# Optimization experiments

Measured on AMD Instinct MI355X. Metric: run time of the kernel, lower is better.

The kernel has to match this reference:

```python
import jax, jax.numpy as jnp
import numpy as np

BN_EPS = 1e-5

def setup_inputs() -> dict:
    key = jax.random.key(0)
    k0, k1, k2, k3, k4 = jax.random.split(key, 5)
    B, N, D, E = 8, 256, 128, 4096
    x_l = jax.random.normal(k0, (B, N, D), dtype=jnp.float32)
    src = jax.random.randint(k1, (E,), 0, N)
    dst = jax.random.randint(k2, (E,), 0, N)
    edge_index_l = jnp.stack([src, dst], axis=0)  # [2, E]
    mask_l = jax.random.randint(k3, (B, N), 0, 2).astype(bool)
    W = jax.random.normal(k4, (D, D), dtype=jnp.float32) * (1.0 / np.sqrt(D))
    b = jnp.zeros((D,), jnp.float32)
    gamma = jnp.ones((D,), jnp.float32)
    beta = jnp.zeros((D,), jnp.float32)
    return {"x_l": x_l, "edge_index_l": edge_index_l, "mask_l": mask_l,
            "W": W, "b": b, "gamma": gamma, "beta": beta}


def reference(x_l, edge_index_l, mask_l, W, b, gamma, beta):
    # x_l: [B, N, D]; edge_index_l: [2, E]; mask_l: [B, N] bool
    B, N, D = x_l.shape
    src, dst = edge_index_l[0], edge_index_l[1]
    # Vectorized replacement of the Python edge loop: edges with dst - src == 3
    # zero the mask at both endpoints (the explicit interaction zeroing in the
    # original is subsumed by the mask, since masked entries never survive).
    cov = (dst - src) == 3  # [E] bool
    hit = jnp.zeros((N,), bool)
    hit = hit.at[src].max(cov)
    hit = hit.at[dst].max(cov)
    mask = mask_l & ~hit[None, :]  # [B, N]
    # Pairwise mask: outer AND minus diagonal
    eye = jnp.eye(N, dtype=bool)
    pair_mask = (mask[:, :, None] & mask[:, None, :]) & ~eye[None]  # [B, N, N]
    # Outer-product interaction: [B, N, N, D]
    interaction = x_l[:, :, None, :] * x_l[:, None, :, :]
    # Linear
    h = jnp.einsum('bijd,ed->bije', interaction, W) + b
    # BatchNorm1d over the masked (selected) rows, training-mode batch stats.
    m = pair_mask[..., None].astype(h.dtype)  # [B, N, N, 1]
    cnt = jnp.maximum(jnp.sum(m), 1.0)
    mean = jnp.sum(h * m, axis=(0, 1, 2)) / cnt  # [D]
    var = jnp.sum(m * (h - mean) ** 2, axis=(0, 1, 2)) / cnt  # biased, as torch BN
    hn = (h - mean) * jax.lax.rsqrt(var + BN_EPS) * gamma + beta
    # Dropout is identity in eval mode; LeakyReLU slope 0.01 (torch default).
    out = jax.nn.leaky_relu(hn, negative_slope=0.01) * m  # zero non-selected entries
    return out, pair_mask
```

## Files before the change

kernel.cpp:

```cpp
#include <hip/hip_runtime.h>

#define B_ 8
#define N_ 256
#define D_ 128
#define E_ 4096

typedef __attribute__((ext_vector_type(8))) short bf16x8;
typedef __attribute__((ext_vector_type(4))) float f32x4;
typedef __attribute__((ext_vector_type(2))) float f32x2;

__device__ inline unsigned int pack2bf(float lo, float hi) {
    unsigned ul = __float_as_uint(lo);
    ul = ul + 0x7FFFu + ((ul >> 16) & 1u);
    unsigned uh = __float_as_uint(hi);
    uh = uh + 0x7FFFu + ((uh >> 16) & 1u);
    return (ul >> 16) | (uh & 0xFFFF0000u);
}

__device__ inline unsigned short f2bf(float f) {
    unsigned u = __float_as_uint(f);
    u = u + 0x7FFFu + ((u >> 16) & 1u);
    return (unsigned short)(u >> 16);
}


__global__ __launch_bounds__(256) void k_prep(const void* __restrict__ edges_raw,
                                              const void* __restrict__ mask_raw,
                                              const float* __restrict__ W,
                                              int* __restrict__ mask,
                                              int* __restrict__ jlist,
                                              int* __restrict__ jcnt,
                                              unsigned short* __restrict__ Wb,
                                              float* __restrict__ Wt,
                                              float* __restrict__ tq,
                                              float* __restrict__ dq) {
    int blk = blockIdx.x, tid = threadIdx.x;
    if (blk >= B_) {
        int idx = (blk - B_) * 256 + tid;
        if (idx < 16384) {
            float w = W[idx];
            Wb[idx] = f2bf(w);
            int e = idx >> 7, d = idx & 127;
            Wt[d * D_ + e] = w;
        } else if (idx < 16512) tq[idx - 16384] = 0.0f;
        else dq[idx - 16512] = 0.0f;
        return;
    }
    int b = blk;
    __shared__ unsigned char hit[N_];
    __shared__ int flags[2];
    __shared__ int wcnt[4], wbase[4];
    hit[tid] = 0;
    if (tid < 2) flags[tid] = 0;
    __syncthreads();

    const unsigned char* mb = (const unsigned char*)mask_raw;
    int loc_m = 0;
    for (int idx = tid; idx < B_ * N_; idx += 256)
        if ((idx & 3) && mb[idx]) loc_m = 1;
    if (loc_m) flags[0] = 1;
    const int* e32 = (const int*)edges_raw;
    int loc_e = 0;
    for (int idx = tid; idx < 2 * E_; idx += 256)
        if ((idx & 1) && e32[idx]) loc_e = 1;
    if (loc_e) flags[1] = 1;
    __syncthreads();

    int mask_is_u8 = flags[0], e_is_i32 = flags[1];
    const long long* e64 = (const long long*)edges_raw;
    for (int e = tid; e < E_; e += 256) {
        int s, d;
        if (e_is_i32) { s = e32[e]; d = e32[E_ + e]; }
        else          { s = (int)e64[e]; d = (int)e64[E_ + e]; }
        if (d - s == 3) { hit[s] = 1; hit[d] = 1; }
    }
    __syncthreads();

    const int* m32 = (const int*)mask_raw;
    int lane = tid & 63, wid = tid >> 6;
    int raw = mask_is_u8 ? (int)(mb[b * N_ + tid] != 0) : (int)(m32[b * N_ + tid] != 0);
    int m = raw && (hit[tid] == 0);
    mask[b * N_ + tid] = m;
    unsigned long long bal = __ballot(m);
    if (lane == 0) wcnt[wid] = __popcll(bal);
    __syncthreads();
    if (tid == 0) {
        int base = 0;
        for (int w = 0; w < 4; ++w) { wbase[w] = base; base += wcnt[w]; }
        jcnt[b] = base;
    }
    __syncthreads();
    if (m) {
        int pos = wbase[wid] + __popcll(bal & ((1ull << lane) - 1ull));
        jlist[b * N_ + pos] = tid;
    }
}

__global__ __launch_bounds__(128) void k_gram3(const float* __restrict__ x,
                                               const int* __restrict__ jlist,
                                               const int* __restrict__ jcnt,
                                               float* __restrict__ part,
                                               float* __restrict__ s1,
                                               float* __restrict__ cdiag) {
    int d = blockIdx.x, b = blockIdx.y, dp = threadIdx.x;
    int kc = jcnt[b];
    const int* jl = jlist + b * N_;
    const float* xb = x + (size_t)b * N_ * D_;
    float c0 = 0, c1 = 0, q0 = 0, q1 = 0, s0 = 0, s1a = 0;
    int t = 0;
    for (; t + 1 < kc; t += 2) {
        int i0 = jl[t], i1 = jl[t + 1];
        float xd0 = xb[i0 * D_ + d], xp0 = xb[i0 * D_ + dp];
        float xd1 = xb[i1 * D_ + d], xp1 = xb[i1 * D_ + dp];
        c0 += xd0 * xp0; q0 += (xd0 * xd0) * (xp0 * xp0); s0 += xd0;
        c1 += xd1 * xp1; q1 += (xd1 * xd1) * (xp1 * xp1); s1a += xd1;
    }
    if (t < kc) {
        int i0 = jl[t];
        float xd0 = xb[i0 * D_ + d], xp0 = xb[i0 * D_ + dp];
        c0 += xd0 * xp0; q0 += (xd0 * xd0) * (xp0 * xp0); s0 += xd0;
    }
    float c = c0 + c1, q = q0 + q1, sa = s0 + s1a;
    part[((size_t)b * D_ + d) * D_ + dp] = c * c - q;
    if (dp == d) cdiag[b * D_ + d] = c;
    if (dp == 0) s1[b * D_ + d] = sa;
}

__global__ __launch_bounds__(128) void k_mw2(const float* __restrict__ part,
                                             const float* __restrict__ Wt,
                                             const float* __restrict__ s1,
                                             const float* __restrict__ cdiag,
                                             float* __restrict__ tq,
                                             float* __restrict__ dq) {
    __shared__ float Ms[D_];
    __shared__ float svs;
    int d = blockIdx.x, e = threadIdx.x;
    float m = 0.0f;
#pragma unroll
    for (int b = 0; b < B_; ++b) m += part[((size_t)b * D_ + d) * D_ + e];
    Ms[e] = m;
    if (e == 0) {
        float sv = 0.0f;
#pragma unroll
        for (int b = 0; b < B_; ++b) {
            float s = s1[b * D_ + d];
            sv += s * s - cdiag[b * D_ + d];
        }
        svs = sv;
    }
    __syncthreads();
    float y = 0.0f;
#pragma unroll 8
    for (int p = 0; p < D_; ++p) y += Ms[p] * Wt[p * D_ + e];
    float wed = Wt[d * D_ + e];
    atomicAdd(tq + e, wed * y);
    atomicAdd(dq + e, wed * svs);
}

__global__ __launch_bounds__(256) void k_mega(const float* __restrict__ x,
                                              const int* __restrict__ mask,
                                              const int* __restrict__ jlist,
                                              const int* __restrict__ jcnt,
                                              const unsigned short* __restrict__ Wb,
                                              const float* __restrict__ tq,
                                              const float* __restrict__ dq,
                                              const float* __restrict__ bvec,
                                              const float* __restrict__ gamma,
                                              const float* __restrict__ beta,
                                              float* __restrict__ out,
                                              float* __restrict__ pair) {
    __shared__ int msk[N_];
    __shared__ int jls[N_];
    __shared__ __align__(16) unsigned char Vsb[32 * 256];
    __shared__ float scs[D_], shs[D_];

    int blk = blockIdx.x, tid = threadIdx.x;
    int q5 = blk / 5;
    f32x4 z4 = (f32x4)(0.f);

    if (blk != q5 * 5) {
        int zblk = blk - q5 - 1;
        int r0 = zblk * 64;
        int j0 = r0 & 255;
        int i = (r0 >> 8) & 255;
        int b = r0 >> 16;
        int mi = mask[b * N_ + i];
        f32x4* outrow = (f32x4*)(out + (size_t)(b * N_ + i) * N_ * D_);
        int c = tid & 31, g = tid >> 5;
#pragma unroll
        for (int p = 0; p < 8; ++p) {
            int j = j0 + g + 8 * p;
            int mj = mask[b * N_ + j];
            if (!mi || !mj || j == i)
                __builtin_nontemporal_store(z4, &outrow[(size_t)j * 32 + c]);
        }
        return;
    }

    int cblk = q5;
    int b = cblk >> 8, i = cblk & 255;
    int mi = mask[b * N_ + i];

    if (!mi) {
        __builtin_nontemporal_store(0.0f, &pair[(size_t)(b * N_ + i) * N_ + tid]);
        return;
    }

    msk[tid] = mask[b * N_ + tid];
    jls[tid] = jlist[b * N_ + tid];

    if (tid < D_) {
        float cnt = 0.0f;
#pragma unroll
        for (int bb = 0; bb < B_; ++bb) {
            float k = (float)jcnt[bb];
            cnt += k * k - k;
        }
        if (cnt < 1.0f) cnt = 1.0f;
        float be = bvec[tid];
        float mean = dq[tid] / cnt + be;
        float eh2 = tq[tid] / cnt + 2.0f * be * mean - be * be;
        float var = eh2 - mean * mean;
        if (var < 0.0f) var = 0.0f;
        float s = gamma[tid] * rsqrtf(var + 1e-5f);
        scs[tid] = s;
        shs[tid] = be * s + beta[tid] - mean * s;
    }
    __syncthreads();

    float pm = (msk[tid] && tid != i) ? 1.0f : 0.0f;
    __builtin_nontemporal_store(pm, &pair[(size_t)(b * N_ + i) * N_ + tid]);

    int w = tid >> 6, l = tid & 63;
    int lo16 = l & 15, hi4 = l >> 4;
    int E0 = w * 32;

    bf16x8 bfrag[2][4];
#pragma unroll
    for (int et = 0; et < 2; ++et) {
        int e = E0 + 2 * lo16 + et;
#pragma unroll
        for (int ks = 0; ks < 4; ++ks)
            bfrag[et][ks] = *(const bf16x8*)(Wb + (size_t)e * D_ + ks * 32 + hi4 * 8);
    }

    float sc0 = scs[E0 + 2 * lo16], sh0 = shs[E0 + 2 * lo16];
    float sc1 = scs[E0 + 2 * lo16 + 1], sh1 = shs[E0 + 2 * lo16 + 1];

    int kc = jcnt[b];
    const float* xi = x + (size_t)(b * N_ + i) * D_;
    const float* xb = x + (size_t)b * N_ * D_;
    float* outbase = out + (size_t)(b * N_ + i) * N_ * D_;

    for (int jt = 0; jt < kc; jt += 32) {
        __syncthreads();
        int jn = kc - jt; if (jn > 32) jn = 32;

        {
            int r = tid >> 3, q = tid & 7;
            int jrow = jt + r;
            bool ok = (r < jn);
            const float* xj = ok ? (xb + (size_t)jls[jrow] * D_) : xi;
            int d0 = q * 16;
            int rx = (r & 7) << 4;
            float4 a0 = *(const float4*)(xj + d0);
            float4 a1 = *(const float4*)(xj + d0 + 4);
            float4 a2 = *(const float4*)(xj + d0 + 8);
            float4 a3 = *(const float4*)(xj + d0 + 12);
            float4 b0 = *(const float4*)(xi + d0);
            float4 b1 = *(const float4*)(xi + d0 + 4);
            float4 b2 = *(const float4*)(xi + d0 + 8);
            float4 b3 = *(const float4*)(xi + d0 + 12);
            uint4 pk1, pk2;
            pk1.x = pack2bf(a0.x * b0.x, a0.y * b0.y);
            pk1.y = pack2bf(a0.z * b0.z, a0.w * b0.w);
            pk1.z = pack2bf(a1.x * b1.x, a1.y * b1.y);
            pk1.w = pack2bf(a1.z * b1.z, a1.w * b1.w);
            pk2.x = pack2bf(a2.x * b2.x, a2.y * b2.y);
            pk2.y = pack2bf(a2.z * b2.z, a2.w * b2.w);
            pk2.z = pack2bf(a3.x * b3.x, a3.y * b3.y);
            pk2.w = pack2bf(a3.z * b3.z, a3.w * b3.w);
            if (!ok) { pk1 = make_uint4(0, 0, 0, 0); pk2 = pk1; }
            *(uint4*)(Vsb + r * 256 + ((2 * d0) ^ rx)) = pk1;
            *(uint4*)(Vsb + r * 256 + ((2 * (d0 + 8)) ^ rx)) = pk2;
        }
        __syncthreads();

#pragma unroll
        for (int jq = 0; jq < 2; ++jq) {
            f32x4 acc0 = (f32x4)(0.f);
            f32x4 acc1 = (f32x4)(0.f);
            int rA = jq * 16 + lo16;
            int rbase = rA * 256;
            int rx = (rA & 7) << 4;
#pragma unroll
            for (int ks = 0; ks < 4; ++ks) {
                bf16x8 afr = *(const bf16x8*)(Vsb + rbase + ((ks * 64 + hi4 * 16) ^ rx));
                acc0 = __builtin_amdgcn_mfma_f32_16x16x32_bf16(afr, bfrag[0][ks], acc0, 0, 0, 0);
                acc1 = __builtin_amdgcn_mfma_f32_16x16x32_bf16(afr, bfrag[1][ks], acc1, 0, 0, 0);
            }
#pragma unroll
            for (int v = 0; v < 4; ++v) {
                int jrow = jt + jq * 16 + hi4 * 4 + v;
                if (jrow < kc) {
                    int j = jls[jrow];
                    if (j != i) {
                        float h0 = acc0[v] * sc0 + sh0;
                        float h1 = acc1[v] * sc1 + sh1;
                        f32x2 o;
                        o.x = h0 >= 0.f ? h0 : 0.01f * h0;
                        o.y = h1 >= 0.f ? h1 : 0.01f * h1;
                        __builtin_nontemporal_store(o,
                            (f32x2*)(outbase + (size_t)j * D_ + E0 + 2 * lo16));
                    }
                }
            }
        }
    }
}

extern "C" void kernel_launch(void* const* d_in, const int* in_sizes, int n_in,
                              void* d_out, int out_size, void* d_ws, size_t ws_size,
                              hipStream_t stream) {
    const float* x = (const float*)d_in[0];
    const void* edges = d_in[1];
    const void* mask_in = d_in[2];
    const float* W = (const float*)d_in[3];
    const float* bvec = (const float*)d_in[4];
    const float* gamma = (const float*)d_in[5];
    const float* beta = (const float*)d_in[6];

    float* out = (float*)d_out;
    float* pair = out + (size_t)B_ * N_ * N_ * D_;

    char* ws = (char*)d_ws;
    int* mask = (int*)(ws + 0);
    int* jlist = (int*)(ws + 8192);
    int* jcnt = (int*)(ws + 16384);
    float* tq = (float*)(ws + 16448);
    float* dq = (float*)(ws + 16960);
    unsigned short* Wb = (unsigned short*)(ws + 17472);
    float* Wt = (float*)(ws + 50240);
    float* s1 = (float*)(ws + 115776);
    float* cdiag = (float*)(ws + 119872);
    float* part = (float*)(ws + 123968);

    k_prep<<<73, 256, 0, stream>>>(edges, mask_in, W, mask, jlist, jcnt, Wb, Wt, tq, dq);
    {
        dim3 g(D_, B_);
        k_gram3<<<g, 128, 0, stream>>>(x, jlist, jcnt, part, s1, cdiag);
    }
    k_mw2<<<128, 128, 0, stream>>>(part, Wt, s1, cdiag, tq, dq);
    k_mega<<<10240, 256, 0, stream>>>(x, mask, jlist, jcnt, Wb, tq, dq,
                                      bvec, gamma, beta, out, pair);
}
```

Before: 94.84 us.

## Compute all j per row densely instead of compacted jlist plus zero-fill blocks

Replaces the split design, where one compute block per row handled only the compacted valid j list and four extra blocks per row zero-filled the masked entries. Each block now owns one full (b,i) row: masked rows store zeros for the whole row, and valid rows run the MFMA over all 256 j and multiply by the pair mask before storing. This removes the 5x block count, the jlist indirection and the separate zero pass, and makes every output store contiguous. In exchange it spends MFMA and conversion work on masked j, roughly half the pairs. It also hoists the x_i loads out of the tile loop and adds a launch-bounds occupancy hint.

New measurement: 98.77 us. 4.1% more time.

```diff
diff --git a/kernel.cpp b/kernel.cpp
--- a/kernel.cpp
+++ b/kernel.cpp
@@ -157,57 +157,36 @@
     atomicAdd(dq + e, wed * svs);
 }
 
-__global__ __launch_bounds__(256) void k_mega(const float* __restrict__ x,
-                                              const int* __restrict__ mask,
-                                              const int* __restrict__ jlist,
-                                              const int* __restrict__ jcnt,
-                                              const unsigned short* __restrict__ Wb,
-                                              const float* __restrict__ tq,
-                                              const float* __restrict__ dq,
-                                              const float* __restrict__ bvec,
-                                              const float* __restrict__ gamma,
-                                              const float* __restrict__ beta,
-                                              float* __restrict__ out,
-                                              float* __restrict__ pair) {
+__global__ __launch_bounds__(256, 4) void k_mega(const float* __restrict__ x,
+                                                 const int* __restrict__ mask,
+                                                 const int* __restrict__ jcnt,
+                                                 const unsigned short* __restrict__ Wb,
+                                                 const float* __restrict__ tq,
+                                                 const float* __restrict__ dq,
+                                                 const float* __restrict__ bvec,
+                                                 const float* __restrict__ gamma,
+                                                 const float* __restrict__ beta,
+                                                 float* __restrict__ out,
+                                                 float* __restrict__ pair) {
     __shared__ int msk[N_];
-    __shared__ int jls[N_];
     __shared__ __align__(16) unsigned char Vsb[32 * 256];
     __shared__ float scs[D_], shs[D_];
 
     int blk = blockIdx.x, tid = threadIdx.x;
-    int q5 = blk / 5;
+    int b = blk >> 8, i = blk & 255;
+    int mi = mask[b * N_ + i];
     f32x4 z4 = (f32x4)(0.f);
-
-    if (blk != q5 * 5) {
-        int zblk = blk - q5 - 1;
-        int r0 = zblk * 64;
-        int j0 = r0 & 255;
-        int i = (r0 >> 8) & 255;
-        int b = r0 >> 16;
-        int mi = mask[b * N_ + i];
-        f32x4* outrow = (f32x4*)(out + (size_t)(b * N_ + i) * N_ * D_);
-        int c = tid & 31, g = tid >> 5;
-#pragma unroll
-        for (int p = 0; p < 8; ++p) {
-            int j = j0 + g + 8 * p;
-            int mj = mask[b * N_ + j];
-            if (!mi || !mj || j == i)
-                __builtin_nontemporal_store(z4, &outrow[(size_t)j * 32 + c]);
-        }
-        return;
-    }
-
-    int cblk = q5;
-    int b = cblk >> 8, i = cblk & 255;
-    int mi = mask[b * N_ + i];
+    f32x4* outrow = (f32x4*)(out + (size_t)(b * N_ + i) * N_ * D_);
 
     if (!mi) {
         __builtin_nontemporal_store(0.0f, &pair[(size_t)(b * N_ + i) * N_ + tid]);
+#pragma unroll
+        for (int p = 0; p < 32; ++p)
+            __builtin_nontemporal_store(z4, &outrow[tid + 256 * p]);
         return;
     }
 
     msk[tid] = mask[b * N_ + tid];
-    jls[tid] = jlist[b * N_ + tid];
 
     if (tid < D_) {
         float cnt = 0.0f;
@@ -247,40 +226,36 @@
     float sc0 = scs[E0 + 2 * lo16], sh0 = shs[E0 + 2 * lo16];
     float sc1 = scs[E0 + 2 * lo16 + 1], sh1 = shs[E0 + 2 * lo16 + 1];
 
-    int kc = jcnt[b];
     const float* xi = x + (size_t)(b * N_ + i) * D_;
+    int d0 = (tid & 7) * 16;
+    float4 bx0 = *(const float4*)(xi + d0);
+    float4 bx1 = *(const float4*)(xi + d0 + 4);
+    float4 bx2 = *(const float4*)(xi + d0 + 8);
+    float4 bx3 = *(const float4*)(xi + d0 + 12);
+
     const float* xb = x + (size_t)b * N_ * D_;
     float* outbase = out + (size_t)(b * N_ + i) * N_ * D_;
 
-    for (int jt = 0; jt < kc; jt += 32) {
+    for (int jt = 0; jt < N_; jt += 32) {
         __syncthreads();
-        int jn = kc - jt; if (jn > 32) jn = 32;
 
         {
-            int r = tid >> 3, q = tid & 7;
-            int jrow = jt + r;
-            bool ok = (r < jn);
-            const float* xj = ok ? (xb + (size_t)jls[jrow] * D_) : xi;
-            int d0 = q * 16;
+            int r = tid >> 3;
+            const float* xj = xb + (size_t)(jt + r) * D_;
             int rx = (r & 7) << 4;
             float4 a0 = *(const float4*)(xj + d0);
             float4 a1 = *(const float4*)(xj + d0 + 4);
             float4 a2 = *(const float4*)(xj + d0 + 8);
             float4 a3 = *(const float4*)(xj + d0 + 12);
-            float4 b0 = *(const float4*)(xi + d0);
-            float4 b1 = *(const float4*)(xi + d0 + 4);
-            float4 b2 = *(const float4*)(xi + d0 + 8);
-            float4 b3 = *(const float4*)(xi + d0 + 12);
             uint4 pk1, pk2;
-            pk1.x = pack2bf(a0.x * b0.x, a0.y * b0.y);
-            pk1.y = pack2bf(a0.z * b0.z, a0.w * b0.w);
-            pk1.z = pack2bf(a1.x * b1.x, a1.y * b1.y);
-            pk1.w = pack2bf(a1.z * b1.z, a1.w * b1.w);
-            pk2.x = pack2bf(a2.x * b2.x, a2.y * b2.y);
-            pk2.y = pack2bf(a2.z * b2.z, a2.w * b2.w);
-            pk2.z = pack2bf(a3.x * b3.x, a3.y * b3.y);
-            pk2.w = pack2bf(a3.z * b3.z, a3.w * b3.w);
-            if (!ok) { pk1 = make_uint4(0, 0, 0, 0); pk2 = pk1; }
+            pk1.x = pack2bf(a0.x * bx0.x, a0.y * bx0.y);
+            pk1.y = pack2bf(a0.z * bx0.z, a0.w * bx0.w);
+            pk1.z = pack2bf(a1.x * bx1.x, a1.y * bx1.y);
+            pk1.w = pack2bf(a1.z * bx1.z, a1.w * bx1.w);
+            pk2.x = pack2bf(a2.x * bx2.x, a2.y * bx2.y);
+            pk2.y = pack2bf(a2.z * bx2.z, a2.w * bx2.w);
+            pk2.z = pack2bf(a3.x * bx3.x, a3.y * bx3.y);
+            pk2.w = pack2bf(a3.z * bx3.z, a3.w * bx3.w);
             *(uint4*)(Vsb + r * 256 + ((2 * d0) ^ rx)) = pk1;
             *(uint4*)(Vsb + r * 256 + ((2 * (d0 + 8)) ^ rx)) = pk2;
         }
@@ -301,19 +276,15 @@
             }
 #pragma unroll
             for (int v = 0; v < 4; ++v) {
-                int jrow = jt + jq * 16 + hi4 * 4 + v;
-                if (jrow < kc) {
-                    int j = jls[jrow];
-                    if (j != i) {
-                        float h0 = acc0[v] * sc0 + sh0;
-                        float h1 = acc1[v] * sc1 + sh1;
-                        f32x2 o;
-                        o.x = h0 >= 0.f ? h0 : 0.01f * h0;
-                        o.y = h1 >= 0.f ? h1 : 0.01f * h1;
-                        __builtin_nontemporal_store(o,
-                            (f32x2*)(outbase + (size_t)j * D_ + E0 + 2 * lo16));
-                    }
-                }
+                int j = jt + jq * 16 + hi4 * 4 + v;
+                float pmj = (msk[j] && j != i) ? 1.0f : 0.0f;
+                float h0 = acc0[v] * sc0 + sh0;
+                float h1 = acc1[v] * sc1 + sh1;
+                f32x2 o;
+                o.x = (h0 >= 0.f ? h0 : 0.01f * h0) * pmj;
+                o.y = (h1 >= 0.f ? h1 : 0.01f * h1) * pmj;
+                __builtin_nontemporal_store(o,
+                    (f32x2*)(outbase + (size_t)j * D_ + E0 + 2 * lo16));
             }
         }
     }
@@ -351,6 +322,6 @@
         k_gram3<<<g, 128, 0, stream>>>(x, jlist, jcnt, part, s1, cdiag);
     }
     k_mw2<<<128, 128, 0, stream>>>(part, Wt, s1, cdiag, tq, dq);
-    k_mega<<<10240, 256, 0, stream>>>(x, mask, jlist, jcnt, Wb, tq, dq,
-                                      bvec, gamma, beta, out, pair);
-}
+    k_mega<<<B_ * N_, 256, 0, stream>>>(x, mask, jcnt, Wb, tq, dq,
+                                        bvec, gamma, beta, out, pair);
+}
```
